# Performance work log

Measured on AMD Instinct MI355X. Metric: run time of the kernel, lower is better.

## Reference

```python
import jax, jax.numpy as jnp
from jax import lax
import numpy as np

LEVELS = 17
VAR_N = 4
UNITS = 3 * LEVELS          # 51 neurons: motor 17, command 13, inter 21
MOTOR = LEVELS
PRED_N = 4
UNFOLDS = 6                 # ncps LTC default ode_unfolds
EPS = 1e-8
B = 32768                   # recurrence length = B + PRED_N
D = VAR_N * LEVELS          # 68


def _build_wiring(seed=0):
    # AutoNCP(51, 17, sparsity_level=0.8): inter=21, command=13, motor=17
    # sensory_fanout=4, inter_fanout=2, 5 recurrent command synapses, motor_fanin=2
    rng = np.random.default_rng(seed)
    motor, command, S = 17, 13, LEVELS
    N = UNITS
    cmd = np.arange(motor, motor + command)
    intr = np.arange(motor + command, N)
    adj = np.zeros((N, N), np.float32)
    sadj = np.zeros((S, N), np.float32)
    pol = lambda: float(rng.choice([-1.0, 1.0]))
    for s in range(S):
        for d in rng.choice(intr, 4, replace=False):
            sadj[s, d] = pol()
    for d in intr:
        if not sadj[:, d].any():
            sadj[int(rng.integers(S)), d] = pol()
    for i in intr:
        for d in rng.choice(cmd, 2, replace=False):
            adj[i, d] = pol()
    for d in cmd:
        if not adj[intr, d].any():
            adj[int(rng.choice(intr)), d] = pol()
    for _ in range(5):
        adj[int(rng.choice(cmd)), int(rng.choice(cmd))] = pol()
    for m in range(motor):
        for srci in rng.choice(cmd, 2, replace=False):
            adj[srci, m] = pol()
    return adj, sadj


def setup_inputs():
    key = jax.random.key(0)
    ks = iter(jax.random.split(key, 48))
    u = lambda s, lo, hi: jax.random.uniform(next(ks), s, jnp.float32, lo, hi)
    lin = lambda i, o: jax.random.normal(next(ks), (i, o), jnp.float32) * (i ** -0.5)
    adj, sadj = _build_wiring()
    V, N, S = VAR_N, UNITS, LEVELS
    M1 = (LEVELS + D) // 2           # 42
    G = VAR_N * D                    # 272
    G2 = (G + D) // 2                # 170
    return dict(
        x=jax.random.normal(next(ks), (B, D), jnp.float32),
        pre_w1=lin(D, D), pre_b1=jnp.zeros((D,), jnp.float32),
        pre_w2=lin(D, D), pre_b2=jnp.zeros((D,), jnp.float32),
        gleak=u((V, N), 0.001, 1.0), vleak=u((V, N), -0.2, 0.2), cm=u((V, N), 0.4, 0.6),
        w=u((V, N, N), 0.001, 1.0), sigma=u((V, N, N), 3.0, 8.0), mu=u((V, N, N), 0.3, 0.8),
        erev=jnp.asarray(np.tile(adj, (V, 1, 1))),
        sens_w=u((V, S, N), 0.001, 1.0), sens_sigma=u((V, S, N), 3.0, 8.0), sens_mu=u((V, S, N), 0.3, 0.8),
        sens_erev=jnp.asarray(np.tile(sadj, (V, 1, 1))),
        in_w=jnp.ones((V, S), jnp.float32), in_b=jnp.zeros((V, S), jnp.float32),
        out_w=jnp.ones((V, MOTOR), jnp.float32), out_b=jnp.zeros((V, MOTOR), jnp.float32),
        tW1=lin(LEVELS, LEVELS), tb1=jnp.zeros((LEVELS,), jnp.float32),
        tW2=lin(LEVELS, M1), tb2=jnp.zeros((M1,), jnp.float32),
        tW3=lin(M1, D), tb3=jnp.zeros((D,), jnp.float32),
        gW1=lin(G, G), gb1=jnp.zeros((G,), jnp.float32),
        gW2=lin(G, G2), gb2=jnp.zeros((G2,), jnp.float32),
        gW3=lin(G2, D), gb3=jnp.zeros((D,), jnp.float32),
        mask=jnp.asarray((adj != 0).astype(np.float32)),
        sens_mask=jnp.asarray((sadj != 0).astype(np.float32)),
    )


def _forward(x, pre_w1, pre_b1, pre_w2, pre_b2,
             gleak, vleak, cm, w, sigma, mu, erev,
             sens_w, sens_sigma, sens_mu, sens_erev,
             in_w, in_b, out_w, out_b,
             tW1, tb1, tW2, tb2, tW3, tb3,
             gW1, gb1, gW2, gb2, gW3, gb3,
             mask, sens_mask, ckpt=False):
    sig = jax.nn.sigmoid
    # VarEncoder: Linear -> Sigmoid -> Linear
    h = sig(x @ pre_w1 + pre_b1) @ pre_w2 + pre_b2                  # (B, 68)
    xs = h.reshape(-1, VAR_N, LEVELS).transpose(1, 0, 2)            # (V, B, 17)
    seqs = jnp.concatenate([xs, jnp.repeat(xs[:, -1:, :], PRED_N, axis=1)], axis=1)  # (V, T, 17)

    def run(p, seq):
        gl_, vl_, cm_, w_, sg_, mu_, er_, sw_, ssg_, smu_, ser_, iw_, ib_, ow_, ob_ = p
        gl = jax.nn.softplus(gl_)                 # (N,)
        wp = jax.nn.softplus(w_) * mask           # (N, N) sparse NCP wiring
        swp = jax.nn.softplus(sw_) * sens_mask    # (S, N)
        cmt = jax.nn.softplus(cm_) * UNFOLDS      # cm / (elapsed=1 / unfolds)

        def step(v, u_in):
            u = u_in * iw_ + ib_                                   # affine input mapping
            sact = swp * sig((u[:, None] - smu_) * ssg_)           # (S, N)
            num_s = (sact * ser_).sum(0)
            den_s = sact.sum(0)

            def unfold(vv, _):
                wa = wp * sig((vv[:, None] - mu_) * sg_)           # (N, N), src axis 0
                vv = (cmt * vv + gl * vl_ + (wa * er_).sum(0) + num_s) / (
                    cmt + gl + wa.sum(0) + den_s + EPS)
                return vv, None

            v, _ = lax.scan(unfold, v, None, length=UNFOLDS)
            return v, v[:MOTOR] * ow_ + ob_                        # affine output mapping

        stepf = jax.checkpoint(step) if ckpt else step
        _, outs = lax.scan(stepf, jnp.zeros((UNITS,), seq.dtype), seq)
        return outs                                                # (T, 17)

    p = (gleak, vleak, cm, w, sigma, mu, erev,
         sens_w, sens_sigma, sens_mu, sens_erev, in_w, in_b, out_w, out_b)
    rs = jax.vmap(run, in_axes=(0, 0))(p, seqs)                    # (V, T, 17)
    r = rs.transpose(1, 0, 2)                                      # (T, V, 17)
    # CrossConnector: per-tile MLP 17->17->42->68 (sigmoids), flatten, 272->272->170->68
    t = sig(sig(sig(r @ tW1 + tb1) @ tW2 + tb2) @ tW3 + tb3)        # (T, V, 68)
    g = t.reshape(t.shape[0], -1)                                   # (T, 272)
    return sig(sig(g @ gW1 + gb1) @ gW2 + gb2) @ gW3 + gb3          # (T, 68)


def reference(x, pre_w1, pre_b1, pre_w2, pre_b2,
              gleak, vleak, cm, w, sigma, mu, erev,
              sens_w, sens_sigma, sens_mu, sens_erev,
              in_w, in_b, out_w, out_b,
              tW1, tb1, tW2, tb2, tW3, tb3,
              gW1, gb1, gW2, gb2, gW3, gb3,
              mask, sens_mask):
    return _forward(x, pre_w1, pre_b1, pre_w2, pre_b2,
                    gleak, vleak, cm, w, sigma, mu, erev,
                    sens_w, sens_sigma, sens_mu, sens_erev,
                    in_w, in_b, out_w, out_b,
                    tW1, tb1, tW2, tb2, tW3, tb3,
                    gW1, gb1, gW2, gb2, gW3, gb3,
                    mask, sens_mask)
```

## Files before the change

kernel.cpp:

```cpp
#include <hip/hip_runtime.h>
#include <hip/hip_bf16.h>
#include <math.h>

#define LEVELS 17
#define VARN   4
#define UNITS  51
#define MOTOR  17
#define NB     32768
#define TT     (NB + 4)
#define DD     68
#define LOG2E  1.4426950408889634f
#define TROWS  16

#define W_WARM  10
#define L_CHUNK 34
#define NCHUNK  ((TT + L_CHUNK - 1) / L_CHUNK)

#define W_F     64
#define L_F     64
#define NCHUNK_F ((TT + L_F - 1) / L_F)
#define CAP_R  16

#define MROWS  48
#define MBLK   ((TT + MROWS - 1) / MROWS)
#define EBLK   ((NB + MROWS - 1) / MROWS)
#define BUFSZ  (48 * 272 + 64)
#define EBUFSZ (48 * 72 + 64)

#define OFF_WA 0
#define OFF_WB 7680
#define OFF_WC 24576
#define OFF_WD 76800
#define OFF_WE 155136
#define OFF_WF 205824
#define OFF_P1 221184
#define OFF_P2 228864
#define WTS_SHORTS 236544
#define PSENS_N (VARN * LEVELS * UNITS)

typedef __attribute__((ext_vector_type(8))) short short8v;
typedef __attribute__((ext_vector_type(4))) float f32x4;

__device__ __forceinline__ float fast_rcp(float x) { return __builtin_amdgcn_rcpf(x); }
__device__ __forceinline__ float fast_exp2(float x) { return __builtin_amdgcn_exp2f(x); }
__device__ __forceinline__ float sigf(float x) { return fast_rcp(1.0f + __expf(-x)); }
__device__ __forceinline__ float softplusf(float x) { return logf(1.0f + expf(x)); }
__device__ __forceinline__ unsigned short f2bf(float x) {
    unsigned int u = __float_as_uint(x);
    unsigned int r = u + 0x7FFFu + ((u >> 16) & 1u);
    return (unsigned short)(r >> 16);
}

__global__ __launch_bounds__(256) void prep_all(
    const float* __restrict__ tW1, const float* __restrict__ tW2, const float* __restrict__ tW3,
    const float* __restrict__ gW1, const float* __restrict__ gW2, const float* __restrict__ gW3,
    const float* __restrict__ pW1, const float* __restrict__ pW2,
    const float* __restrict__ sens_w, const float* __restrict__ sens_sigma,
    const float* __restrict__ sens_mu, const float* __restrict__ sens_erev,
    unsigned short* __restrict__ wts, float4* __restrict__ psens)
{
    const int ph = blockIdx.y;
    if (ph == 8) {
        int idx = blockIdx.x * 256 + threadIdx.x;
        if (idx >= PSENS_N) return;
        float sg = sens_sigma[idx], m = sens_mu[idx];
        float wf = softplusf(sens_w[idx]);
        psens[idx] = make_float4(fast_exp2(sg * m * LOG2E), -sg * LOG2E, wf, wf * sens_erev[idx]);
        return;
    }
    const int KTt[8]   = {3, 3, 6, 9, 9, 6, 3, 3};
    const int NCt[8]   = {5, 11, 17, 17, 11, 5, 5, 5};
    const int offsT[8] = {OFF_WA, OFF_WB, OFF_WC, OFF_WD, OFF_WE, OFF_WF, OFF_P1, OFF_P2};
    int S = NCt[ph] * KTt[ph] * 512;
    int idx = blockIdx.x * 256 + threadIdx.x;
    if (idx >= S) return;
    int tile = idx >> 9;
    int r    = idx & 511;
    int lane = r >> 3;
    int e    = r & 7;
    int KTp  = KTt[ph];
    int ct   = tile / KTp;
    int kt   = tile - ct * KTp;
    int n = ct * 16 + (lane & 15);
    int k = kt * 32 + (lane >> 4) * 8 + e;
    float val = 0.0f;
    switch (ph) {
        case 0: if (k < 68 && n < 68) { int v = k / 17; if (n / 17 == v) val = tW1[(k % 17) * 17 + (n % 17)]; } break;
        case 1: if (k < 68 && n < 168) { int v = k / 17; int c = n - 42 * v; if (c >= 0 && c < 42) val = tW2[(k % 17) * 42 + c]; } break;
        case 2: if (k < 168 && n < 272) { int v = k / 42; int c = n - 68 * v; if (c >= 0 && c < 68) val = tW3[(k % 42) * 68 + c]; } break;
        case 3: if (k < 272 && n < 272) val = gW1[k * 272 + n]; break;
        case 4: if (k < 272 && n < 170) val = gW2[k * 170 + n]; break;
        case 5: if (k < 170 && n < 68)  val = gW3[k * 68 + n]; break;
        case 6: if (k < 68 && n < 68)   val = pW1[k * 68 + n]; break;
        case 7: if (k < 68 && n < 68)   val = pW2[k * 68 + n]; break;
    }
    wts[offsT[ph] + idx] = f2bf(val);
}

template<int KT, int NC>
__device__ __forceinline__ void mfma_phase(
    const unsigned short* __restrict__ wt,
    const unsigned short* __restrict__ bufIn, int ldkIn,
    unsigned short* __restrict__ bufOut, int ldkOut,
    const float* __restrict__ bias, int bmod, int Nvalid,
    int lane, int wave)
{
    #pragma unroll
    for (int rt = 0; rt < 3; ++rt) {
        short8v af[KT];
        int abase = (rt * 16 + (lane & 15)) * ldkIn + 8 * (lane >> 4);
        #pragma unroll
        for (int kt = 0; kt < KT; ++kt)
            af[kt] = *reinterpret_cast<const short8v*>(&bufIn[abase + kt * 32]);
        for (int ct = wave; ct < NC; ct += 4) {
            int c = ct * 16 + (lane & 15);
            const unsigned short* wp = wt + (size_t)(ct * KT) * 512 + lane * 8;
            short8v bf[KT];
            #pragma unroll
            for (int kt = 0; kt < KT; ++kt)
                bf[kt] = *reinterpret_cast<const short8v*>(&wp[kt * 512]);
            f32x4 acc = {0.0f, 0.0f, 0.0f, 0.0f};
            #pragma unroll
            for (int kt = 0; kt < KT; ++kt)
                acc = __builtin_amdgcn_mfma_f32_16x16x32_bf16(af[kt], bf[kt], acc, 0, 0, 0);
            float bv = 0.0f;
            if (c < Nvalid) {
                int cb = (bmod == 0) ? (c % 17) : (bmod == 1) ? (c % 42) : (bmod == 2) ? (c % 68) : c;
                bv = bias[cb];
            }
            #pragma unroll
            for (int i = 0; i < 4; ++i) {
                float vv = sigf(acc[i] + bv);
                int rl = rt * 16 + (lane >> 4) * 4 + i;
                if (c < ldkOut) bufOut[rl * ldkOut + c] = f2bf(vv);
            }
        }
    }
}

template<int KT>
__device__ __forceinline__ void mfma_final(
    const unsigned short* __restrict__ wt,
    const unsigned short* __restrict__ bufIn, int ldkIn,
    float* __restrict__ io, int baseRow,
    const float* __restrict__ gb3, int lane, int wave)
{
    #pragma unroll
    for (int rt = 0; rt < 3; ++rt) {
        short8v af[KT];
        int abase = (rt * 16 + (lane & 15)) * ldkIn + 8 * (lane >> 4);
        #pragma unroll
        for (int kt = 0; kt < KT; ++kt)
            af[kt] = *reinterpret_cast<const short8v*>(&bufIn[abase + kt * 32]);
        for (int ct = wave; ct < 5; ct += 4) {
            int c = ct * 16 + (lane & 15);
            const unsigned short* wp = wt + (size_t)(ct * KT) * 512 + lane * 8;
            short8v bf[KT];
            #pragma unroll
            for (int kt = 0; kt < KT; ++kt)
                bf[kt] = *reinterpret_cast<const short8v*>(&wp[kt * 512]);
            f32x4 acc = {0.0f, 0.0f, 0.0f, 0.0f};
            #pragma unroll
            for (int kt = 0; kt < KT; ++kt)
                acc = __builtin_amdgcn_mfma_f32_16x16x32_bf16(af[kt], bf[kt], acc, 0, 0, 0);
            float bv = (c < 68) ? gb3[c] : 0.0f;
            #pragma unroll
            for (int i = 0; i < 4; ++i) {
                int row = baseRow + rt * 16 + (lane >> 4) * 4 + i;
                if (c < 68 && row < TT) io[(size_t)row * DD + c] = acc[i] + bv;
            }
        }
    }
}

__global__ __launch_bounds__(256) void mlp_mfma(
    float* __restrict__ io, const unsigned short* __restrict__ wts,
    const float* __restrict__ tb1, const float* __restrict__ tb2, const float* __restrict__ tb3,
    const float* __restrict__ gb1, const float* __restrict__ gb2, const float* __restrict__ gb3)
{
    __shared__ unsigned short buf0[BUFSZ];
    __shared__ unsigned short buf1[BUFSZ];
    int tid = threadIdx.x, lane = tid & 63, wave = tid >> 6;
    int baseRow = blockIdx.x * MROWS;

    for (int e = tid; e < BUFSZ; e += 256) { buf0[e] = 0; buf1[e] = 0; }
    __syncthreads();
    for (int e = tid; e < MROWS * DD; e += 256) {
        int r = e / DD, c = e % DD;
        int gr = baseRow + r;
        float xv = (gr < TT) ? io[(size_t)gr * DD + c] : 0.0f;
        buf0[r * 72 + c] = f2bf(xv);
    }
    __syncthreads();
    mfma_phase<3, 5 >(wts + OFF_WA, buf0, 72,  buf1, 72,  tb1, 0, 68,  lane, wave); __syncthreads();
    mfma_phase<3, 11>(wts + OFF_WB, buf1, 72,  buf0, 168, tb2, 1, 168, lane, wave); __syncthreads();
    mfma_phase<6, 17>(wts + OFF_WC, buf0, 168, buf1, 272, tb3, 2, 272, lane, wave); __syncthreads();
    mfma_phase<9, 17>(wts + OFF_WD, buf1, 272, buf0, 272, gb1, 3, 272, lane, wave); __syncthreads();
    mfma_phase<9, 11>(wts + OFF_WE, buf0, 272, buf1, 176, gb2, 3, 170, lane, wave); __syncthreads();
    mfma_final<6>(wts + OFF_WF, buf1, 176, io, baseRow, gb3, lane, wave);
}

__global__ __launch_bounds__(256) void enc_mfma(
    const float* __restrict__ x, const unsigned short* __restrict__ wts,
    const float* __restrict__ pb1, const float* __restrict__ pb2,
    float* __restrict__ seq)
{
    __shared__ unsigned short buf0[EBUFSZ];
    __shared__ unsigned short buf1[EBUFSZ];
    int tid = threadIdx.x, lane = tid & 63, wave = tid >> 6;
    int baseRow = blockIdx.x * MROWS;

    for (int e = tid; e < EBUFSZ; e += 256) { buf0[e] = 0; buf1[e] = 0; }
    __syncthreads();
    for (int e = tid; e < MROWS * DD; e += 256) {
        int r = e / DD, c = e % DD;
        int gr = baseRow + r;
        float xv = (gr < NB) ? x[(size_t)gr * DD + c] : 0.0f;
        buf0[r * 72 + c] = f2bf(xv);
    }
    __syncthreads();
    mfma_phase<3, 5>(wts + OFF_P1, buf0, 72, buf1, 72, pb1, 3, 68, lane, wave);
    __syncthreads();
    #pragma unroll
    for (int rt = 0; rt < 3; ++rt) {
        short8v af[3];
        int abase = (rt * 16 + (lane & 15)) * 72 + 8 * (lane >> 4);
        #pragma unroll
        for (int kt = 0; kt < 3; ++kt)
            af[kt] = *reinterpret_cast<const short8v*>(&buf1[abase + kt * 32]);
        for (int ct = wave; ct < 5; ct += 4) {
            int c = ct * 16 + (lane & 15);
            const unsigned short* wp = wts + OFF_P2 + (size_t)(ct * 3) * 512 + lane * 8;
            short8v bf[3];
            #pragma unroll
            for (int kt = 0; kt < 3; ++kt)
                bf[kt] = *reinterpret_cast<const short8v*>(&wp[kt * 512]);
            f32x4 acc = {0.0f, 0.0f, 0.0f, 0.0f};
            #pragma unroll
            for (int kt = 0; kt < 3; ++kt)
                acc = __builtin_amdgcn_mfma_f32_16x16x32_bf16(af[kt], bf[kt], acc, 0, 0, 0);
            float bv = (c < 68) ? pb2[c] : 0.0f;
            #pragma unroll
            for (int i = 0; i < 4; ++i) {
                int row = baseRow + rt * 16 + (lane >> 4) * 4 + i;
                if (c < 68 && row < NB) {
                    float vv = acc[i] + bv;
                    int v = c / 17, s = c % 17;
                    float* dst = seq + ((size_t)v * TT + row) * LEVELS + s;
                    dst[0] = vv;
                    if (row == NB - 1) {
                        dst[1 * LEVELS] = vv; dst[2 * LEVELS] = vv;
                        dst[3 * LEVELS] = vv; dst[4 * LEVELS] = vv;
                    }
                }
            }
        }
    }
}

#define SENS_TPW 16
__global__ __launch_bounds__(256) void sens_kernel(
    const float* __restrict__ seq,
    const float4* __restrict__ psens,
    const float* __restrict__ in_w, const float* __restrict__ in_b,
    const float* __restrict__ sens_mask,
    float2* __restrict__ tab)
{
    int gwi = blockIdx.x * 4 + (threadIdx.x >> 6);
    int j   = threadIdx.x & 63;
    int v    = gwi & 3;
    int tbase = (gwi >> 2) * SENS_TPW;
    if (tbase >= TT) return;

    unsigned int bits0 = 0;
    if (j < UNITS)
        for (int s = 0; s < LEVELS; ++s)
            bits0 |= (sens_mask[s * UNITS + j] != 0.0f ? 1u : 0u) << s;
    int ns = __popc(bits0);
    int mS = ns;
    #pragma unroll
    for (int off = 32; off; off >>= 1) mS = max(mS, __shfl_xor(mS, off, 64));

    float iw = (j < LEVELS) ? in_w[v * LEVELS + j] : 0.0f;
    float ib = (j < LEVELS) ? in_b[v * LEVELS + j] : 0.0f;

    int tend = min(TT, tbase + SENS_TPW);
    for (int t = tbase; t < tend; ++t) {
        float u = (j < LEVELS)
            ? fmaf(seq[((size_t)v * TT + t) * LEVELS + j], iw, ib) : 0.0f;
        unsigned int bits = bits0;
        float num = 0.0f, den = 0.0f;
        for (int k = 0; k < mS; ++k) {
            bool on = (k < ns) && (bits != 0u);
            int s = on ? (__ffs(bits) - 1) : 0;
            if (on) bits &= bits - 1;
            float us = __shfl(u, s, 64);
            float4 p = psens[(v * LEVELS + s) * UNITS + (j < UNITS ? j : 0)];
            float g = fast_rcp(fmaf(p.x, fast_exp2(p.y * us), 1.0f));
            if (on) { num = fmaf(p.w, g, num); den = fmaf(p.z, g, den); }
        }
        if (j < UNITS)
            tab[((size_t)v * TT + t) * UNITS + j] = make_float2(num, den);
    }
}

template<int MH>
__device__ void scan_body3(
    int j, int jnS, int jnV, float ownMul, float helpMul, int h1, int h2,
    int myStart, int myCnt, bool isH1,
    unsigned long long colbits, int v, int t0, int wstart, int tend,
    float cmt, float glvl, float cgl, float ow, float ob,
    const float* __restrict__ w, const float* __restrict__ sigma,
    const float* __restrict__ mu, const float* __restrict__ erev,
    const float2* __restrict__ tab, float* __restrict__ rout)
{
    int   src[MH]; float fw[MH], fc[MH], fk[MH], fwfe[MH];
    unsigned long long bits = colbits;
    for (int s = 0; s < myStart; ++s) bits &= bits - 1;
    #pragma unroll
    for (int k = 0; k < MH; ++k) {
        bool on = (k < myCnt);
        int sc = on ? (__ffsll((unsigned long long)bits) - 1) : 0;
        src[k] = sc;
        size_t pi = ((size_t)v * UNITS + sc) * UNITS + jnS;
        float sg = on ? sigma[pi] : 0.0f;
        float m  = on ? mu[pi]    : 0.0f;
        fw[k] = on ? softplusf(w[pi]) : 0.0f;
        fc[k] = fast_exp2(sg * m * LOG2E);
        fk[k] = -sg * LOG2E;
        fwfe[k] = on ? fw[k] * erev[pi] : 0.0f;
        if (on) bits &= bits - 1;
    }
    const float2* tp = tab + (size_t)v * TT * UNITS + jnV;
    float* rp = rout + (size_t)v * LEVELS + j;
    float2 nd = tp[(size_t)t0 * UNITS];
    float vreg = 0.0f;
    for (int t = t0; t < tend; ++t) {
        float2 ndc = nd;
        if (t + 1 < tend) nd = tp[(size_t)(t + 1) * UNITS];
        float bn = isH1 ? 0.0f : (glvl + ndc.x);
        float bd = isH1 ? 1.0f : (cgl + ndc.y);
        #pragma unroll
        for (int uf = 0; uf < 6; ++uf) {
            float vs[MH];
            #pragma unroll
            for (int k = 0; k < MH; ++k) vs[k] = __shfl(vreg, src[k], 64);
            float accn = 0.0f, accd = 0.0f;
            #pragma unroll
            for (int k = 0; k < MH; ++k) {
                float g = fast_rcp(fmaf(fc[k], fast_exp2(fk[k] * vs[k]), 1.0f));
                accn = fmaf(fwfe[k], g, accn);
                accd = fmaf(fw[k], g, accd);
            }
            float p1n = __shfl(accn, h1, 64);
            float p1d = __shfl(accd, h1, 64);
            float p2n = __shfl(accn, h2, 64);
            float p2d = __shfl(accd, h2, 64);
            float num = fmaf(accn, ownMul, bn) + helpMul * (p1n + p2n);
            float den = fmaf(accd, ownMul, bd) + helpMul * (p1d + p2d);
            vreg = fmaf(cmt, vreg, num) * fast_rcp(den);
        }
        if (j < MOTOR && t >= wstart) rp[(size_t)t * DD] = fmaf(vreg, ow, ob);
    }
}

__device__ void scan_body_gen(
    int j, int jn, bool hasHelp, int partner, int myStart, int myCnt, int mcMax,
    unsigned long long colbits, int v, int t0, int wstart, int tend,
    float cmt, float glvl, float cgl, float ow, float ob, bool isHelper,
    const float* __restrict__ w, const float* __restrict__ sigma,
    const float* __restrict__ mu, const float* __restrict__ erev,
    const float2* __restrict__ tab, float* __restrict__ rout)
{
    unsigned long long mybits = colbits;
    for (int s = 0; s < myStart; ++s) mybits &= mybits - 1;
    const float2* tp = tab + (size_t)v * TT * UNITS + jn;
    float* rp = rout + (size_t)v * LEVELS + j;
    float vreg = 0.0f;
    for (int t = t0; t < tend; ++t) {
        float2 ndc = tp[(size_t)t * UNITS];
        float bn = isHelper ? 0.0f : (glvl + ndc.x);
        float bd = isHelper ? 0.0f : (cgl + ndc.y);
        for (int uf = 0; uf < 6; ++uf) {
            unsigned long long bits = mybits;
            float num = bn, den = bd;
            for (int k = 0; k < mcMax; ++k) {
                bool on = (k < myCnt) && (bits != 0ull);
                int sc = on ? (__ffsll(bits) - 1) : 0;
                if (on) bits &= bits - 1;
                float vs = __shfl(vreg, sc, 64);
                size_t pi = ((size_t)v * UNITS + sc) * UNITS + jn;
                float a = on ? softplusf(w[pi]) * sigf((vs - mu[pi]) * sigma[pi]) : 0.0f;
                num = fmaf(a, on ? erev[pi] : 0.0f, num);
                den += a;
            }
            float pn = __shfl(num, partner, 64);
            float pd = __shfl(den, partner, 64);
            if (hasHelp) { num += pn; den += pd; }
            vreg = fmaf(cmt, vreg, num) * fast_rcp(den);
        }
        if (j < MOTOR && t >= wstart) rp[(size_t)t * DD] = fmaf(vreg, ow, ob);
    }
}

__global__ __launch_bounds__(256, 8) void scan_pre(
    const float2* __restrict__ tab,
    const float* __restrict__ gleak, const float* __restrict__ vleak, const float* __restrict__ cm,
    const float* __restrict__ w, const float* __restrict__ sigma,
    const float* __restrict__ mu, const float* __restrict__ erev,
    const float* __restrict__ out_w, const float* __restrict__ out_b,
    const float* __restrict__ mask,
    float* __restrict__ rout)
{
    int gwi = (blockIdx.x << 2) + (threadIdx.x >> 6);
    int j = threadIdx.x & 63;
    int v = gwi & 3;
    int chunk = gwi >> 2;
    if (chunk >= NCHUNK) return;
    int wstart = chunk * L_CHUNK;
    int tend = min(TT, wstart + L_CHUNK);
    int t0 = max(0, wstart - W_WARM);

    bool isH1   = (j >= UNITS);
    bool isH2   = (j >= 30 && j < 43);
    bool isCmdL = (j >= MOTOR && j < 30);
    int jnV = isH1 ? (j - 34) : j;
    int jnS = isH1 ? (j - 34) : (isH2 ? (j - 13) : j);

    unsigned long long colbits = 0ull;
    for (int i = 0; i < UNITS; ++i)
        colbits |= (unsigned long long)(mask[i * UNITS + jnS] != 0.0f ? 1 : 0) << i;
    int nf = __popcll(colbits);

    int ownIn = 0;
    if (j >= 30 && j < UNITS) {
        for (int i = 0; i < UNITS; ++i)
            ownIn |= (mask[i * UNITS + j] != 0.0f ? 1 : 0);
    }
    int bad = ownIn;
    #pragma unroll
    for (int off = 32; off; off >>= 1) bad |= __shfl_xor(bad, off, 64);

    int n1 = (nf + 2) / 3;
    int n2 = (nf - n1 + 1) / 2;
    int n3 = nf - n1 - n2;
    int myStart, myCnt;
    if (isH1)        { myStart = n1 + n2; myCnt = n3; }
    else if (isH2)   { myStart = n1;      myCnt = n2; }
    else if (isCmdL) { myStart = 0;       myCnt = n1; }
    else             { myStart = 0;       myCnt = nf; }
    float ownMul  = (isH1 || isH2) ? 0.0f : 1.0f;
    float helpMul = isCmdL ? 1.0f : 0.0f;
    int h1 = isCmdL ? (j + 34) : j;
    int h2 = isCmdL ? (j + 13) : j;

    float cmt  = softplusf(cm[v * UNITS + jnV]) * 6.0f;
    float gl   = softplusf(gleak[v * UNITS + jnV]);
    float glvl = gl * vleak[v * UNITS + jnV];
    float cgl  = cmt + gl + 1e-8f;
    float ow = (j < MOTOR) ? out_w[v * LEVELS + j] : 0.0f;
    float ob = (j < MOTOR) ? out_b[v * LEVELS + j] : 0.0f;

    int mc = myCnt;
    #pragma unroll
    for (int off = 32; off; off >>= 1) mc = max(mc, __shfl_xor(mc, off, 64));

    if (!bad && mc <= 2)
        scan_body3<2>(j, jnS, jnV, ownMul, helpMul, h1, h2, myStart, myCnt, isH1,
                      colbits, v, t0, wstart, tend, cmt, glvl, cgl, ow, ob,
                      w, sigma, mu, erev, tab, rout);
    else if (!bad && mc <= 3)
        scan_body3<3>(j, jnS, jnV, ownMul, helpMul, h1, h2, myStart, myCnt, isH1,
                      colbits, v, t0, wstart, tend, cmt, glvl, cgl, ow, ob,
                      w, sigma, mu, erev, tab, rout);
    else if (!bad && mc <= 4)
        scan_body3<4>(j, jnS, jnV, ownMul, helpMul, h1, h2, myStart, myCnt, isH1,
                      colbits, v, t0, wstart, tend, cmt, glvl, cgl, ow, ob,
                      w, sigma, mu, erev, tab, rout);
    else {
        int jn = isH1 ? (j - 34) : j;
        unsigned long long cb = 0ull;
        for (int i = 0; i < UNITS; ++i)
            cb |= (unsigned long long)(mask[i * UNITS + jn] != 0.0f ? 1 : 0) << i;
        int nfg = __popcll(cb);
        bool isCmd = (jn >= MOTOR && jn < 30);
        int nh = (nfg + 1) >> 1;
        int gs, gc;
        if (isH1)      { gs = nh; gc = nfg - nh; }
        else if (isCmd){ gs = 0;  gc = nh; }
        else           { gs = 0;  gc = nfg; }
        bool hasHelp = (!isH1) && isCmd;
        int partner = hasHelp ? (jn + 34) : j;
        float cmtg  = softplusf(cm[v * UNITS + jn]) * 6.0f;
        float glg   = softplusf(gleak[v * UNITS + jn]);
        float glvlg = glg * vleak[v * UNITS + jn];
        float cglg  = cmtg + glg + 1e-8f;
        int mg = gc;
        #pragma unroll
        for (int off = 32; off; off >>= 1) mg = max(mg, __shfl_xor(mg, off, 64));
        scan_body_gen(j, jn, hasHelp, partner, gs, gc, mg, cb, v, t0, wstart, tend,
                      cmtg, glvlg, cglg, ow, ob, isH1, w, sigma, mu, erev, tab, rout);
    }
}

__global__ __launch_bounds__(128) void enc_kernel(
    const float* __restrict__ x,
    const float* __restrict__ W1, const float* __restrict__ b1,
    const float* __restrict__ W2, const float* __restrict__ b2,
    float* __restrict__ seq)
{
    int t = blockIdx.x;
    int j = threadIdx.x;
    __shared__ float xs[DD];
    __shared__ float h1[DD];
    if (j < DD) xs[j] = x[(size_t)t * DD + j];
    __syncthreads();
    if (j < DD) {
        float acc = b1[j];
        #pragma unroll 4
        for (int k = 0; k < DD; ++k) acc = fmaf(xs[k], W1[k * DD + j], acc);
        h1[j] = sigf(acc);
    }
    __syncthreads();
    if (j < DD) {
        float acc = b2[j];
        #pragma unroll 4
        for (int k = 0; k < DD; ++k) acc = fmaf(h1[k], W2[k * DD + j], acc);
        int v = j / LEVELS, s = j % LEVELS;
        float* dst = seq + ((size_t)v * TT + t) * LEVELS + s;
        dst[0] = acc;
        if (t == NB - 1) {
            dst[1 * LEVELS] = acc; dst[2 * LEVELS] = acc;
            dst[3 * LEVELS] = acc; dst[4 * LEVELS] = acc;
        }
    }
}

template<int MF, int MS>
__device__ __forceinline__ void scan_loop_f(
    int j, int v, int t0, int wstart, int tend,
    const float* __restrict__ seq, float* __restrict__ rout,
    float cmt, float glvl, float cgl, float iw, float ib, float ow, float ob,
    int nf, int ns,
    const int* rs_, const float* rw_, const float* rc_, const float* rk_, const float* re_,
    const int* ss_, const float* sw_, const float* sc_, const float* sk_, const float* se_)
{
    int fs[MF]; float fw[MF], fc[MF], fk[MF], fe[MF];
    #pragma unroll
    for (int k = 0; k < MF; ++k) {
        bool on = k < nf;
        int idx = j * CAP_R + k;
        fs[k] = on ? rs_[idx] : 0;
        fw[k] = on ? rw_[idx] : 0.0f;
        fc[k] = on ? rc_[idx] : 1.0f;
        fk[k] = on ? rk_[idx] : 0.0f;
        fe[k] = on ? re_[idx] : 0.0f;
    }
    int gs[MS]; float gw[MS], gc[MS], gk[MS], ge[MS];
    #pragma unroll
    for (int k = 0; k < MS; ++k) {
        bool on = k < ns;
        int idx = j * LEVELS + k;
        gs[k] = on ? ss_[idx] : 0;
        gw[k] = on ? sw_[idx] : 0.0f;
        gc[k] = on ? sc_[idx] : 1.0f;
        gk[k] = on ? sk_[idx] : 0.0f;
        ge[k] = on ? se_[idx] : 0.0f;
    }
    const float* sp = seq + (size_t)v * TT * LEVELS + j;
    float* rp = rout + (size_t)v * LEVELS + j;
    float xnext = (j < LEVELS) ? sp[(size_t)t0 * LEVELS] : 0.0f;
    float vreg = 0.0f;
    for (int t = t0; t < tend; ++t) {
        float u = fmaf(xnext, iw, ib);
        if (j < LEVELS && t + 1 < tend) xnext = sp[(size_t)(t + 1) * LEVELS];
        float us[MS];
        #pragma unroll
        for (int k = 0; k < MS; ++k) us[k] = __shfl(u, gs[k], 64);
        float sa[MS];
        #pragma unroll
        for (int k = 0; k < MS; ++k)
            sa[k] = gw[k] * fast_rcp(fmaf(gc[k], fast_exp2(gk[k] * us[k]), 1.0f));
        float bn = glvl, bd = cgl;
        #pragma unroll
        for (int k = 0; k < MS; ++k) { bn = fmaf(sa[k], ge[k], bn); bd += sa[k]; }
        #pragma unroll
        for (int uf = 0; uf < 6; ++uf) {
            float vsa[MF];
            #pragma unroll
            for (int k = 0; k < MF; ++k) vsa[k] = __shfl(vreg, fs[k], 64);
            float aa[MF];
            #pragma unroll
            for (int k = 0; k < MF; ++k)
                aa[k] = fw[k] * fast_rcp(fmaf(fc[k], fast_exp2(fk[k] * vsa[k]), 1.0f));
            float num = bn, den = bd;
            #pragma unroll
            for (int k = 0; k < MF; ++k) { num = fmaf(aa[k], fe[k], num); den += aa[k]; }
            vreg = fmaf(cmt, vreg, num) * fast_rcp(den);
        }
        if (j < LEVELS && t >= wstart) rp[(size_t)t * DD] = fmaf(vreg, ow, ob);
    }
}

__global__ __launch_bounds__(64) void scan_fallback(
    const float* __restrict__ seq,
    const float* __restrict__ gleak, const float* __restrict__ vleak, const float* __restrict__ cm,
    const float* __restrict__ w, const float* __restrict__ sigma,
    const float* __restrict__ mu, const float* __restrict__ erev,
    const float* __restrict__ sens_w, const float* __restrict__ sens_sigma,
    const float* __restrict__ sens_mu, const float* __restrict__ sens_erev,
    const float* __restrict__ in_w, const float* __restrict__ in_b,
    const float* __restrict__ out_w, const float* __restrict__ out_b,
    const float* __restrict__ mask, const float* __restrict__ sens_mask,
    float* __restrict__ rout)
{
    __shared__ int   rs_[UNITS * CAP_R];
    __shared__ float rw_[UNITS * CAP_R], rc_[UNITS * CAP_R], rk_[UNITS * CAP_R], re_[UNITS * CAP_R];
    __shared__ int   ss_[UNITS * LEVELS];
    __shared__ float sw_[UNITS * LEVELS], sc_[UNITS * LEVELS], sk_[UNITS * LEVELS], se_[UNITS * LEVELS];
    __shared__ int   cnts[64], scnts[64];
    __shared__ int   red[2];

    int j = threadIdx.x;
    int v = blockIdx.x & 3;
    int chunk = blockIdx.x >> 2;
    int wstart = chunk * L_F;
    if (wstart >= TT) return;
    int tend = min(TT, wstart + L_F);
    int t0 = max(0, wstart - W_F);

    int nf = 0, ns = 0;
    if (j < UNITS) {
        for (int i = 0; i < UNITS; ++i) {
            if (mask[i * UNITS + j] != 0.0f) {
                if (nf < CAP_R) {
                    size_t pi = ((size_t)v * UNITS + i) * UNITS + j;
                    int idx = j * CAP_R + nf;
                    float sg = sigma[pi], m = mu[pi];
                    rs_[idx] = i;
                    rw_[idx] = softplusf(w[pi]);
                    rc_[idx] = fast_exp2(sg * m * LOG2E);
                    rk_[idx] = -sg * LOG2E;
                    re_[idx] = erev[pi];
                }
                nf++;
            }
        }
        for (int s = 0; s < LEVELS; ++s) {
            if (sens_mask[s * UNITS + j] != 0.0f) {
                size_t pi = ((size_t)v * LEVELS + s) * UNITS + j;
                int idx = j * LEVELS + ns;
                float sg = sens_sigma[pi], m = sens_mu[pi];
                ss_[idx] = s;
                sw_[idx] = softplusf(sens_w[pi]);
                sc_[idx] = fast_exp2(sg * m * LOG2E);
                sk_[idx] = -sg * LOG2E;
                se_[idx] = sens_erev[pi];
                ns++;
            }
        }
    }
    cnts[j] = nf; scnts[j] = ns;
    __syncthreads();
    if (j == 0) {
        int mf = 0, ms = 0;
        for (int i = 0; i < UNITS; ++i) { mf = max(mf, cnts[i]); ms = max(ms, scnts[i]); }
        red[0] = mf; red[1] = ms;
    }
    __syncthreads();
    int maxF = red[0], maxS = red[1];

    int jc = (j < UNITS) ? j : (UNITS - 1);
    float cmt  = softplusf(cm[v * UNITS + jc]) * 6.0f;
    float gl   = softplusf(gleak[v * UNITS + jc]);
    float glvl = gl * vleak[v * UNITS + jc];
    float cgl  = cmt + gl + 1e-8f;
    float iw = (j < LEVELS) ? in_w[v * LEVELS + j]  : 0.0f;
    float ib = (j < LEVELS) ? in_b[v * LEVELS + j]  : 0.0f;
    float ow = (j < LEVELS) ? out_w[v * LEVELS + j] : 0.0f;
    float ob = (j < LEVELS) ? out_b[v * LEVELS + j] : 0.0f;

    if (maxF <= 11 && maxS <= 12)
        scan_loop_f<11, 12>(j, v, t0, wstart, tend, seq, rout, cmt, glvl, cgl, iw, ib, ow, ob, nf, ns,
                            rs_, rw_, rc_, rk_, re_, ss_, sw_, sc_, sk_, se_);
    else
        scan_loop_f<16, 17>(j, v, t0, wstart, tend, seq, rout, cmt, glvl, cgl, iw, ib, ow, ob, nf, ns,
                            rs_, rw_, rc_, rk_, re_, ss_, sw_, sc_, sk_, se_);
}

__global__ __launch_bounds__(256) void mlp_kernel(
    float* __restrict__ io,
    const float* __restrict__ tW1, const float* __restrict__ tb1,
    const float* __restrict__ tW2, const float* __restrict__ tb2,
    const float* __restrict__ tW3, const float* __restrict__ tb3,
    const float* __restrict__ gW1, const float* __restrict__ gb1,
    const float* __restrict__ gW2, const float* __restrict__ gb2,
    const float* __restrict__ gW3, const float* __restrict__ gb3)
{
    __shared__ __align__(16) float A[TROWS][272];
    __shared__ __align__(16) float Bf[TROWS][272];
    int base = blockIdx.x * TROWS;
    int tid = threadIdx.x;

    for (int e = tid; e < TROWS * DD; e += 256) {
        int r = e / DD, c = e % DD;
        A[r][c] = (base + r < TT) ? io[(size_t)(base + r) * DD + c] : 0.0f;
    }
    __syncthreads();
    for (int c = tid; c < 4 * LEVELS; c += 256) {
        int vv = c / LEVELS, cc = c % LEVELS;
        float acc[TROWS]; float bias = tb1[cc];
        #pragma unroll
        for (int r = 0; r < TROWS; ++r) acc[r] = bias;
        for (int k = 0; k < LEVELS; ++k) {
            float wv = tW1[k * LEVELS + cc];
            #pragma unroll
            for (int r = 0; r < TROWS; ++r) acc[r] = fmaf(A[r][vv * LEVELS + k], wv, acc[r]);
        }
        #pragma unroll
        for (int r = 0; r < TROWS; ++r) Bf[r][c] = sigf(acc[r]);
    }
    __syncthreads();
    for (int c = tid; c < 4 * 42; c += 256) {
        int vv = c / 42, cc = c % 42;
        float acc[TROWS]; float bias = tb2[cc];
        #pragma unroll
        for (int r = 0; r < TROWS; ++r) acc[r] = bias;
        for (int k = 0; k < LEVELS; ++k) {
            float wv = tW2[k * 42 + cc];
            #pragma unroll
            for (int r = 0; r < TROWS; ++r) acc[r] = fmaf(Bf[r][vv * LEVELS + k], wv, acc[r]);
        }
        #pragma unroll
        for (int r = 0; r < TROWS; ++r) A[r][vv * 42 + cc] = sigf(acc[r]);
    }
    __syncthreads();
    for (int c = tid; c < 4 * DD; c += 256) {
        int vv = c / DD, cc = c % DD;
        float acc[TROWS]; float bias = tb3[cc];
        #pragma unroll
        for (int r = 0; r < TROWS; ++r) acc[r] = bias;
        for (int k = 0; k < 42; ++k) {
            float wv = tW3[k * DD + cc];
            #pragma unroll
            for (int r = 0; r < TROWS; ++r) acc[r] = fmaf(A[r][vv * 42 + k], wv, acc[r]);
        }
        #pragma unroll
        for (int r = 0; r < TROWS; ++r) Bf[r][c] = sigf(acc[r]);
    }
    __syncthreads();
    for (int c = tid; c < 272; c += 256) {
        float acc[TROWS]; float bias = gb1[c];
        #pragma unroll
        for (int r = 0; r < TROWS; ++r) acc[r] = bias;
        for (int k = 0; k < 272; k += 4) {
            float w0 = gW1[(k + 0) * 272 + c];
            float w1 = gW1[(k + 1) * 272 + c];
            float w2 = gW1[(k + 2) * 272 + c];
            float w3 = gW1[(k + 3) * 272 + c];
            #pragma unroll
            for (int r = 0; r < TROWS; ++r) {
                float4 g4 = *reinterpret_cast<const float4*>(&Bf[r][k]);
                acc[r] = fmaf(g4.x, w0, fmaf(g4.y, w1, fmaf(g4.z, w2, fmaf(g4.w, w3, acc[r]))));
            }
        }
        #pragma unroll
        for (int r = 0; r < TROWS; ++r) A[r][c] = sigf(acc[r]);
    }
    __syncthreads();
    for (int c = tid; c < 170; c += 256) {
        float acc[TROWS]; float bias = gb2[c];
        #pragma unroll
        for (int r = 0; r < TROWS; ++r) acc[r] = bias;
        for (int k = 0; k < 272; k += 4) {
            float w0 = gW2[(k + 0) * 170 + c];
            float w1 = gW2[(k + 1) * 170 + c];
            float w2 = gW2[(k + 2) * 170 + c];
            float w3 = gW2[(k + 3) * 170 + c];
            #pragma unroll
            for (int r = 0; r < TROWS; ++r) {
                float4 g4 = *reinterpret_cast<const float4*>(&A[r][k]);
                acc[r] = fmaf(g4.x, w0, fmaf(g4.y, w1, fmaf(g4.z, w2, fmaf(g4.w, w3, acc[r]))));
            }
        }
        #pragma unroll
        for (int r = 0; r < TROWS; ++r) Bf[r][c] = sigf(acc[r]);
    }
    __syncthreads();
    for (int c = tid; c < DD; c += 256) {
        float acc[TROWS]; float bias = gb3[c];
        #pragma unroll
        for (int r = 0; r < TROWS; ++r) acc[r] = bias;
        for (int k = 0; k < 168; k += 4) {
            float w0 = gW3[(k + 0) * DD + c];
            float w1 = gW3[(k + 1) * DD + c];
            float w2 = gW3[(k + 2) * DD + c];
            float w3 = gW3[(k + 3) * DD + c];
            #pragma unroll
            for (int r = 0; r < TROWS; ++r) {
                float4 g4 = *reinterpret_cast<const float4*>(&Bf[r][k]);
                acc[r] = fmaf(g4.x, w0, fmaf(g4.y, w1, fmaf(g4.z, w2, fmaf(g4.w, w3, acc[r]))));
            }
        }
        for (int k = 168; k < 170; ++k) {
            float wv = gW3[k * DD + c];
            #pragma unroll
            for (int r = 0; r < TROWS; ++r) acc[r] = fmaf(Bf[r][k], wv, acc[r]);
        }
        #pragma unroll
        for (int r = 0; r < TROWS; ++r)
            if (base + r < TT) io[(size_t)(base + r) * DD + c] = acc[r];
    }
}

extern "C" void kernel_launch(void* const* d_in, const int* in_sizes, int n_in,
                              void* d_out, int out_size, void* d_ws, size_t ws_size,
                              hipStream_t stream)
{
    (void)in_sizes; (void)n_in; (void)out_size;
    const float* x        = (const float*)d_in[0];
    const float* pre_w1   = (const float*)d_in[1];
    const float* pre_b1   = (const float*)d_in[2];
    const float* pre_w2   = (const float*)d_in[3];
    const float* pre_b2   = (const float*)d_in[4];
    const float* gleak    = (const float*)d_in[5];
    const float* vleak    = (const float*)d_in[6];
    const float* cm       = (const float*)d_in[7];
    const float* w        = (const float*)d_in[8];
    const float* sigma    = (const float*)d_in[9];
    const float* mu       = (const float*)d_in[10];
    const float* erev     = (const float*)d_in[11];
    const float* sens_w   = (const float*)d_in[12];
    const float* sens_sig = (const float*)d_in[13];
    const float* sens_mu  = (const float*)d_in[14];
    const float* sens_er  = (const float*)d_in[15];
    const float* in_w     = (const float*)d_in[16];
    const float* in_b     = (const float*)d_in[17];
    const float* out_w    = (const float*)d_in[18];
    const float* out_b    = (const float*)d_in[19];
    const float* tW1      = (const float*)d_in[20];
    const float* tb1      = (const float*)d_in[21];
    const float* tW2      = (const float*)d_in[22];
    const float* tb2      = (const float*)d_in[23];
    const float* tW3      = (const float*)d_in[24];
    const float* tb3      = (const float*)d_in[25];
    const float* gW1      = (const float*)d_in[26];
    const float* gb1      = (const float*)d_in[27];
    const float* gW2      = (const float*)d_in[28];
    const float* gb2      = (const float*)d_in[29];
    const float* gW3      = (const float*)d_in[30];
    const float* gb3      = (const float*)d_in[31];
    const float* mask     = (const float*)d_in[32];
    const float* smask    = (const float*)d_in[33];

    float* out = (float*)d_out;

    size_t tab_bytes = (size_t)VARN * TT * UNITS * sizeof(float2);
    size_t seq_bytes = (size_t)VARN * TT * LEVELS * sizeof(float);
    size_t wts_bytes = (size_t)WTS_SHORTS * sizeof(unsigned short);
    size_t ps_bytes  = (size_t)PSENS_N * sizeof(float4);

    if (ws_size >= tab_bytes + seq_bytes + wts_bytes + ps_bytes) {
        float2* tab = (float2*)d_ws;
        float*  seq = (float*)((char*)d_ws + tab_bytes);
        unsigned short* wts = (unsigned short*)((char*)d_ws + tab_bytes + seq_bytes);
        float4* psens = (float4*)((char*)d_ws + tab_bytes + seq_bytes + wts_bytes);
        prep_all<<<dim3(306, 9), 256, 0, stream>>>(
            tW1, tW2, tW3, gW1, gW2, gW3, pre_w1, pre_w2,
            sens_w, sens_sig, sens_mu, sens_er, wts, psens);
        enc_mfma<<<EBLK, 256, 0, stream>>>(x, wts, pre_b1, pre_b2, seq);
        {
            int slabs = (TT + SENS_TPW - 1) / SENS_TPW;
            int waves = slabs * VARN;
            sens_kernel<<<(waves + 3) / 4, 256, 0, stream>>>(
                seq, psens, in_w, in_b, smask, tab);
        }
        scan_pre<<<NCHUNK, 256, 0, stream>>>(
            tab, gleak, vleak, cm, w, sigma, mu, erev, out_w, out_b, mask, out);
        mlp_mfma<<<MBLK, 256, 0, stream>>>(out, wts, tb1, tb2, tb3, gb1, gb2, gb3);
    } else if (ws_size >= seq_bytes) {
        float* seq = (float*)d_ws;
        enc_kernel<<<NB, 128, 0, stream>>>(x, pre_w1, pre_b1, pre_w2, pre_b2, seq);
        scan_fallback<<<VARN * NCHUNK_F, 64, 0, stream>>>(
            seq, gleak, vleak, cm, w, sigma, mu, erev,
            sens_w, sens_sig, sens_mu, sens_er,
            in_w, in_b, out_w, out_b, mask, smask, out);
        mlp_kernel<<<(TT + TROWS - 1) / TROWS, 256, 0, stream>>>(
            out, tW1, tb1, tW2, tb2, tW3, tb3, gW1, gb1, gW2, gb2, gW3, gb3);
    }
}
```

Measured before the change: 223.0 us.

## Interleave two independent scan chunks per wavefront to expose ILP

```diff
diff --git a/kernel.cpp b/kernel.cpp
--- a/kernel.cpp
+++ b/kernel.cpp
@@ -15,6 +15,7 @@
 #define W_WARM  10
 #define L_CHUNK 34
 #define NCHUNK  ((TT + L_CHUNK - 1) / L_CHUNK)
+#define NPAIR   ((NCHUNK + 1) / 2)
 
 #define W_F     64
 #define L_F     64
@@ -305,10 +306,12 @@
 }
 
 template<int MH>
-__device__ void scan_body3(
+__device__ void scan_body3x2(
     int j, int jnS, int jnV, float ownMul, float helpMul, int h1, int h2,
     int myStart, int myCnt, bool isH1,
-    unsigned long long colbits, int v, int t0, int wstart, int tend,
+    unsigned long long colbits, int v,
+    int t0a, int wstartA, int tendA,
+    int t0b, int wstartB, int tendB,
     float cmt, float glvl, float cgl, float ow, float ob,
     const float* __restrict__ w, const float* __restrict__ sigma,
     const float* __restrict__ mu, const float* __restrict__ erev,
@@ -333,34 +336,53 @@
     }
     const float2* tp = tab + (size_t)v * TT * UNITS + jnV;
     float* rp = rout + (size_t)v * LEVELS + j;
-    float2 nd = tp[(size_t)t0 * UNITS];
-    float vreg = 0.0f;
-    for (int t = t0; t < tend; ++t) {
-        float2 ndc = nd;
-        if (t + 1 < tend) nd = tp[(size_t)(t + 1) * UNITS];
-        float bn = isH1 ? 0.0f : (glvl + ndc.x);
-        float bd = isH1 ? 1.0f : (cgl + ndc.y);
+    int lenA = tendA - t0a;
+    int lenB = tendB - t0b;
+    int iters = max(lenA, lenB);
+    float2 ndA = tp[(size_t)t0a * UNITS];
+    float2 ndB = (lenB > 0) ? tp[(size_t)t0b * UNITS] : make_float2(0.0f, 0.0f);
+    float vA = 0.0f, vB = 0.0f;
+    for (int i = 0; i < iters; ++i) {
+        float2 ncA = ndA;
+        if (i + 1 < lenA) ndA = tp[(size_t)(t0a + i + 1) * UNITS];
+        float2 ncB = ndB;
+        if (i + 1 < lenB) ndB = tp[(size_t)(t0b + i + 1) * UNITS];
+        float bnA = isH1 ? 0.0f : (glvl + ncA.x);
+        float bdA = isH1 ? 1.0f : (cgl + ncA.y);
+        float bnB = isH1 ? 0.0f : (glvl + ncB.x);
+        float bdB = isH1 ? 1.0f : (cgl + ncB.y);
         #pragma unroll
         for (int uf = 0; uf < 6; ++uf) {
-            float vs[MH];
-            #pragma unroll
-            for (int k = 0; k < MH; ++k) vs[k] = __shfl(vreg, src[k], 64);
-            float accn = 0.0f, accd = 0.0f;
+            float vsA[MH], vsB[MH];
+            #pragma unroll
+            for (int k = 0; k < MH; ++k) { vsA[k] = __shfl(vA, src[k], 64); vsB[k] = __shfl(vB, src[k], 64); }
+            float anA = 0.0f, adA = 0.0f, anB = 0.0f, adB = 0.0f;
             #pragma unroll
             for (int k = 0; k < MH; ++k) {
-                float g = fast_rcp(fmaf(fc[k], fast_exp2(fk[k] * vs[k]), 1.0f));
-                accn = fmaf(fwfe[k], g, accn);
-                accd = fmaf(fw[k], g, accd);
-            }
-            float p1n = __shfl(accn, h1, 64);
-            float p1d = __shfl(accd, h1, 64);
-            float p2n = __shfl(accn, h2, 64);
-            float p2d = __shfl(accd, h2, 64);
-            float num = fmaf(accn, ownMul, bn) + helpMul * (p1n + p2n);
-            float den = fmaf(accd, ownMul, bd) + helpMul * (p1d + p2d);
-            vreg = fmaf(cmt, vreg, num) * fast_rcp(den);
-        }
-        if (j < MOTOR && t >= wstart) rp[(size_t)t * DD] = fmaf(vreg, ow, ob);
+                float gA = fast_rcp(fmaf(fc[k], fast_exp2(fk[k] * vsA[k]), 1.0f));
+                float gB = fast_rcp(fmaf(fc[k], fast_exp2(fk[k] * vsB[k]), 1.0f));
+                anA = fmaf(fwfe[k], gA, anA);
+                adA = fmaf(fw[k], gA, adA);
+                anB = fmaf(fwfe[k], gB, anB);
+                adB = fmaf(fw[k], gB, adB);
+            }
+            float p1nA = __shfl(anA, h1, 64), p1dA = __shfl(adA, h1, 64);
+            float p2nA = __shfl(anA, h2, 64), p2dA = __shfl(adA, h2, 64);
+            float p1nB = __shfl(anB, h1, 64), p1dB = __shfl(adB, h1, 64);
+            float p2nB = __shfl(anB, h2, 64), p2dB = __shfl(adB, h2, 64);
+            float numA = fmaf(anA, ownMul, bnA) + helpMul * (p1nA + p2nA);
+            float denA = fmaf(adA, ownMul, bdA) + helpMul * (p1dA + p2dA);
+            float numB = fmaf(anB, ownMul, bnB) + helpMul * (p1nB + p2nB);
+            float denB = fmaf(adB, ownMul, bdB) + helpMul * (p1dB + p2dB);
+            vA = fmaf(cmt, vA, numA) * fast_rcp(denA);
+            vB = fmaf(cmt, vB, numB) * fast_rcp(denB);
+        }
+        if (j < MOTOR) {
+            int ta = t0a + i;
+            if (i < lenA && ta >= wstartA) rp[(size_t)ta * DD] = fmaf(vA, ow, ob);
+            int tb = t0b + i;
+            if (i < lenB && tb >= wstartB) rp[(size_t)tb * DD] = fmaf(vB, ow, ob);
+        }
     }
 }
 
@@ -415,11 +437,18 @@
     int gwi = (blockIdx.x << 2) + (threadIdx.x >> 6);
     int j = threadIdx.x & 63;
     int v = gwi & 3;
-    int chunk = gwi >> 2;
-    if (chunk >= NCHUNK) return;
-    int wstart = chunk * L_CHUNK;
-    int tend = min(TT, wstart + L_CHUNK);
-    int t0 = max(0, wstart - W_WARM);
+    int pr = gwi >> 2;
+    if (pr >= NPAIR) return;
+    int chunkA = 2 * pr;
+    int chunkB = 2 * pr + 1;
+    int wstartA = chunkA * L_CHUNK;
+    if (wstartA >= TT) return;
+    int tendA = min(TT, wstartA + L_CHUNK);
+    int t0a = max(0, wstartA - W_WARM);
+    int wstartB = chunkB * L_CHUNK;
+    bool hasB = (chunkB < NCHUNK) && (wstartB < TT);
+    int tendB = hasB ? min(TT, wstartB + L_CHUNK) : 0;
+    int t0b = hasB ? max(0, wstartB - W_WARM) : 0;
 
     bool isH1   = (j >= UNITS);
     bool isH2   = (j >= 30 && j < 43);
@@ -466,17 +495,17 @@
     for (int off = 32; off; off >>= 1) mc = max(mc, __shfl_xor(mc, off, 64));
 
     if (!bad && mc <= 2)
-        scan_body3<2>(j, jnS, jnV, ownMul, helpMul, h1, h2, myStart, myCnt, isH1,
-                      colbits, v, t0, wstart, tend, cmt, glvl, cgl, ow, ob,
-                      w, sigma, mu, erev, tab, rout);
+        scan_body3x2<2>(j, jnS, jnV, ownMul, helpMul, h1, h2, myStart, myCnt, isH1,
+                        colbits, v, t0a, wstartA, tendA, t0b, wstartB, tendB,
+                        cmt, glvl, cgl, ow, ob, w, sigma, mu, erev, tab, rout);
     else if (!bad && mc <= 3)
-        scan_body3<3>(j, jnS, jnV, ownMul, helpMul, h1, h2, myStart, myCnt, isH1,
-                      colbits, v, t0, wstart, tend, cmt, glvl, cgl, ow, ob,
-                      w, sigma, mu, erev, tab, rout);
+        scan_body3x2<3>(j, jnS, jnV, ownMul, helpMul, h1, h2, myStart, myCnt, isH1,
+                        colbits, v, t0a, wstartA, tendA, t0b, wstartB, tendB,
+                        cmt, glvl, cgl, ow, ob, w, sigma, mu, erev, tab, rout);
     else if (!bad && mc <= 4)
-        scan_body3<4>(j, jnS, jnV, ownMul, helpMul, h1, h2, myStart, myCnt, isH1,
-                      colbits, v, t0, wstart, tend, cmt, glvl, cgl, ow, ob,
-                      w, sigma, mu, erev, tab, rout);
+        scan_body3x2<4>(j, jnS, jnV, ownMul, helpMul, h1, h2, myStart, myCnt, isH1,
+                        colbits, v, t0a, wstartA, tendA, t0b, wstartB, tendB,
+                        cmt, glvl, cgl, ow, ob, w, sigma, mu, erev, tab, rout);
     else {
         int jn = isH1 ? (j - 34) : j;
         unsigned long long cb = 0ull;
@@ -498,8 +527,11 @@
         int mg = gc;
         #pragma unroll
         for (int off = 32; off; off >>= 1) mg = max(mg, __shfl_xor(mg, off, 64));
-        scan_body_gen(j, jn, hasHelp, partner, gs, gc, mg, cb, v, t0, wstart, tend,
+        scan_body_gen(j, jn, hasHelp, partner, gs, gc, mg, cb, v, t0a, wstartA, tendA,
                       cmtg, glvlg, cglg, ow, ob, isH1, w, sigma, mu, erev, tab, rout);
+        if (hasB)
+            scan_body_gen(j, jn, hasHelp, partner, gs, gc, mg, cb, v, t0b, wstartB, tendB,
+                          cmtg, glvlg, cglg, ow, ob, isH1, w, sigma, mu, erev, tab, rout);
     }
 }
 
@@ -875,7 +907,7 @@
             sens_kernel<<<(waves + 3) / 4, 256, 0, stream>>>(
                 seq, psens, in_w, in_b, smask, tab);
         }
-        scan_pre<<<NCHUNK, 256, 0, stream>>>(
+        scan_pre<<<NPAIR, 256, 0, stream>>>(
             tab, gleak, vleak, cm, w, sigma, mu, erev, out_w, out_b, mask, out);
         mlp_mfma<<<MBLK, 256, 0, stream>>>(out, wts, tb1, tb2, tb3, gb1, gb2, gb3);
     } else if (ws_size >= seq_bytes) {
```

New measurement: 239.9 us. 1.08x slower.
